# Kernel optimization log

Hardware: AMD Instinct MI355X
Metric: run time of the kernel (lower is better)

## Reference

```python
import jax, jax.numpy as jnp
import numpy as np

C = 128      # in channels
CO = 64      # out channels
G = 32       # group-norm groups
RES_IN = 32  # input resolution
RES_OUT = 64 # subdivided resolution
N = 20000    # active input voxels
EPS = 1e-5


def setup_inputs() -> dict:
    key = jax.random.key(0)
    ks = jax.random.split(key, 12)
    # unique active voxel coords at RES_IN (batch index 0, single instance)
    rng = np.random.default_rng(0)
    flat = rng.choice(RES_IN ** 3, size=N, replace=False)
    xyz = np.stack([flat // (RES_IN * RES_IN), (flat // RES_IN) % RES_IN, flat % RES_IN], axis=1)
    x_coords = jnp.asarray(np.concatenate([np.zeros((N, 1), np.int32), xyz.astype(np.int32)], axis=1))
    x_feats = jax.random.normal(ks[0], (N, C), dtype=jnp.float32)
    gn1_g = 1.0 + 0.1 * jax.random.normal(ks[1], (C,), dtype=jnp.float32)
    gn1_b = 0.1 * jax.random.normal(ks[2], (C,), dtype=jnp.float32)
    W1 = 0.05 * jax.random.normal(ks[3], (3, 3, 3, C, CO), dtype=jnp.float32)
    b1 = 0.01 * jax.random.normal(ks[4], (CO,), dtype=jnp.float32)
    gn2_g = 1.0 + 0.1 * jax.random.normal(ks[5], (CO,), dtype=jnp.float32)
    gn2_b = 0.1 * jax.random.normal(ks[6], (CO,), dtype=jnp.float32)
    W2 = 0.05 * jax.random.normal(ks[7], (3, 3, 3, CO, CO), dtype=jnp.float32)  # zero_module in source; random here to exercise math
    b2 = 0.01 * jax.random.normal(ks[8], (CO,), dtype=jnp.float32)
    Ws = 0.05 * jax.random.normal(ks[9], (C, CO), dtype=jnp.float32)   # 1x1 skip conv
    bs = 0.01 * jax.random.normal(ks[10], (CO,), dtype=jnp.float32)
    return dict(x_feats=x_feats, x_coords=x_coords, gn1_g=gn1_g, gn1_b=gn1_b,
                W1=W1, b1=b1, gn2_g=gn2_g, gn2_b=gn2_b, W2=W2, b2=b2, Ws=Ws, bs=bs)


def group_norm(f, g, b):
    # single-instance sparse group norm: stats per group over all points
    n, c = f.shape
    x = f.reshape(n, G, c // G)
    mu = jnp.mean(x, axis=(0, 2), keepdims=True)
    var = jnp.mean((x - mu) ** 2, axis=(0, 2), keepdims=True)
    return ((x - mu) * jax.lax.rsqrt(var + EPS)).reshape(n, c) * g + b


def subdivide(coords, feats):
    n = coords.shape[0]
    offs = jnp.stack(jnp.meshgrid(jnp.arange(2), jnp.arange(2), jnp.arange(2), indexing='ij'), -1).reshape(8, 3)
    xyz = coords[:, None, 1:] * 2 + offs[None].astype(coords.dtype)          # [n,8,3]
    bidx = jnp.broadcast_to(coords[:, None, :1], (n, 8, 1))
    new_coords = jnp.concatenate([bidx, xyz], axis=-1).reshape(n * 8, 4)
    return new_coords, jnp.repeat(feats, 8, axis=0)


def subm_conv3(coords, feats, W, b):
    # submanifold 3x3x3 sparse conv: scatter to padded dense grid, gather 27 neighbors per active site
    cin = feats.shape[1]
    grid = jnp.zeros((RES_OUT + 2, RES_OUT + 2, RES_OUT + 2, cin), feats.dtype)
    grid = grid.at[coords[:, 1] + 1, coords[:, 2] + 1, coords[:, 3] + 1].set(feats)
    acc = jnp.zeros((feats.shape[0], W.shape[-1]), feats.dtype)
    for i in range(3):
        for j in range(3):
            for k in range(3):
                nb = grid[coords[:, 1] + i, coords[:, 2] + j, coords[:, 3] + k]  # [n, cin]
                acc = acc + nb @ W[i, j, k]
    return acc + b


def reference(x_feats, x_coords, gn1_g, gn1_b, W1, b1, gn2_g, gn2_b, W2, b2, Ws, bs):
    h = jax.nn.silu(group_norm(x_feats, gn1_g, gn1_b))
    hc, hf = subdivide(x_coords, h)
    _, xf = subdivide(x_coords, x_feats)
    hf = subm_conv3(hc, hf, W1, b1)
    hf = jax.nn.silu(group_norm(hf, gn2_g, gn2_b))
    hf = subm_conv3(hc, hf, W2, b2)
    out = hf + (xf @ Ws + bs)  # residual + 1x1 skip conv (out_channels != channels)
    return out
```

## Files before the change

### kernel.cpp

```cpp
#include <hip/hip_runtime.h>
#include <hip/hip_bf16.h>
#include <math.h>

#define N_PTS 20000
#define C_IN 128
#define C_OUT 64
#define M_PTS (N_PTS*8)
#define EPS 1e-5f

typedef __attribute__((ext_vector_type(8))) short short8;
typedef __attribute__((ext_vector_type(4))) float float4v;

__device__ __forceinline__ ushort f2bf(float f){
    unsigned int i = __float_as_uint(f);
    unsigned int r = i + 0x7fffu + ((i >> 16) & 1u);
    return (ushort)(r >> 16);
}
__device__ __forceinline__ float bf2f(ushort u){ return __uint_as_float(((unsigned int)u) << 16); }
__device__ __forceinline__ float silu(float z){ return z / (1.f + expf(-z)); }


__global__ void __launch_bounds__(256) prep_kernel(
    const float* __restrict__ W1, const float* __restrict__ W2,
    ushort* __restrict__ Wt1, ushort* __restrict__ Wt2,
    int* __restrict__ pg, ushort* __restrict__ h, ushort* __restrict__ h2,
    const float* __restrict__ x, float* __restrict__ stats)
{
    const int b = blockIdx.x, tid = threadIdx.x;
    if (b < 2048){
        int idx = b * 256 + tid;
        int j = idx & 7, l = (idx >> 3) & 63, nb = (idx >> 9) & 3, kb = (idx >> 11) & 3, t = idx >> 13;
        int ci = kb * 32 + (l >> 4) * 8 + j, co = nb * 16 + (l & 15);
        int o = t >> 3, jj = t & 7;
        int ox = (o >> 2) & 1, oy = (o >> 1) & 1, oz = o & 1;
        int jx = (jj >> 2) & 1, jy = (jj >> 1) & 1, jz = jj & 1;
        float s = 0.f;
#pragma unroll
        for (int dx = -1; dx <= 1; dx++){
            if (((ox + dx) >> 1) != ox + jx - 1) continue;
#pragma unroll
            for (int dy = -1; dy <= 1; dy++){
                if (((oy + dy) >> 1) != oy + jy - 1) continue;
#pragma unroll
                for (int dz = -1; dz <= 1; dz++){
                    if (((oz + dz) >> 1) != oz + jz - 1) continue;
                    s += W1[((dx+1)*9 + (dy+1)*3 + (dz+1)) * (C_IN*64) + ci * 64 + co];
                }
            }
        }
        Wt1[idx] = f2bf(s);
    } else if (b < 2480){
        int idx = (b - 2048) * 256 + tid;
        int j = idx & 7, l = (idx >> 3) & 63, nb = (idx >> 9) & 3, kb = (idx >> 11) & 1, t = idx >> 12;
        int ci = kb * 32 + (l >> 4) * 8 + j, co = nb * 16 + (l & 15);
        Wt2[idx] = f2bf(W2[(t * C_OUT + ci) * 64 + co]);
    } else if (b < 2608){
        int i = (b - 2480) * 256 + tid;
        pg[i] = -1;
        if (b == 2480){
            if (tid < C_IN) h[(size_t)N_PTS * C_IN + tid] = 0;
            if (tid < 256){
                h2[(size_t)M_PTS * C_OUT + tid] = 0;
                h2[(size_t)M_PTS * C_OUT + 256 + tid] = 0;
            }
        }
    } else {
        __shared__ float ls[64];
        if (tid < 64) ls[tid] = 0.f;
        __syncthreads();
        const int g = tid & 31;
        const int r0 = (b - 2608) * 8 + (tid >> 5);
        float sum = 0.f, sq = 0.f;
        for (int r = r0; r < N_PTS; r += 4096){
            float4 v = *(const float4*)(x + (size_t)r * C_IN + g * 4);
            sum += v.x + v.y + v.z + v.w;
            sq  += v.x*v.x + v.y*v.y + v.z*v.z + v.w*v.w;
        }
        atomicAdd(&ls[g], sum);
        atomicAdd(&ls[32 + g], sq);
        __syncthreads();
        if (tid < 64) atomicAdd(&stats[tid], ls[tid]);
    }
}

__global__ void __launch_bounds__(256) mid_kernel(
    const int* __restrict__ cds, int* __restrict__ pg,
    const float* __restrict__ x, const float* __restrict__ stats,
    const float* __restrict__ g1, const float* __restrict__ b1, ushort* __restrict__ h,
    const float* __restrict__ Wsk, const float* __restrict__ bsk, float* __restrict__ s)
{
    __shared__ float w[C_IN * C_OUT];
    const int b = blockIdx.x, tid = threadIdx.x;
    if (b < 79){
        int i = b * 256 + tid;
        if (i < N_PTS){
            const int* cd = cds + i * 4;
            pg[(cd[1] * 32 + cd[2]) * 32 + cd[3]] = i;
        }
    } else if (b < 2579){
        int i = ((b - 79) * 256 + tid) * 4;
        int c0 = i & (C_IN - 1);
        int g = c0 >> 2;
        float mu = stats[g] * (1.0f / (N_PTS * 4.0f));
        float var = stats[32 + g] * (1.0f / (N_PTS * 4.0f)) - mu * mu;
        float rs = rsqrtf(var + EPS);
        float4 v = *(const float4*)(x + i);
        ushort4 o;
        o.x = f2bf(silu((v.x - mu) * rs * g1[c0+0] + b1[c0+0]));
        o.y = f2bf(silu((v.y - mu) * rs * g1[c0+1] + b1[c0+1]));
        o.z = f2bf(silu((v.z - mu) * rs * g1[c0+2] + b1[c0+2]));
        o.w = f2bf(silu((v.w - mu) * rs * g1[c0+3] + b1[c0+3]));
        *(ushort4*)(h + i) = o;
    } else {
        for (int j = tid; j < C_IN * C_OUT; j += 256) w[j] = Wsk[j];
        __syncthreads();
        int co = tid & 63, pr = tid >> 6;
        int p = (b - 2579) * 4 + pr;
        const float* xr = x + (size_t)p * C_IN;
        float a = bsk[co];
        for (int cb = 0; cb < C_IN; cb += 4){
            float4 v = *(const float4*)(xr + cb);
            a += v.x * w[(cb+0)*64+co] + v.y * w[(cb+1)*64+co]
               + v.z * w[(cb+2)*64+co] + v.w * w[(cb+3)*64+co];
        }
        s[(size_t)p * C_OUT + co] = a;
    }
}

__global__ void __launch_bounds__(64, 3) conv1_corner(
    const ushort* __restrict__ feat, const int* __restrict__ pg,
    const int* __restrict__ coords, const ushort* __restrict__ Wt,
    const float* __restrict__ bias, ushort* __restrict__ hf1_bf,
    float* __restrict__ statsAcc)
{
    const int l = threadIdx.x;
    const int r16 = l & 15, qd = l >> 4;
    const int bx = blockIdx.x, o = blockIdx.y;

    int p = bx * 64 + l;
    int pc = p < N_PTS ? p : N_PTS - 1;
    int px = coords[pc*4+1], py = coords[pc*4+2], pz = coords[pc*4+3];
    int ex0 = px + ((o >> 2) & 1) - 1;
    int ey0 = py + ((o >> 1) & 1) - 1;
    int ez0 = pz + (o & 1) - 1;

    int rows8[8];
#pragma unroll
    for (int j = 0; j < 8; j++){
        int cx = ex0 + ((j >> 2) & 1), cy = ey0 + ((j >> 1) & 1), cz = ez0 + (j & 1);
        int row = N_PTS;
        if ((unsigned)cx < 32u && (unsigned)cy < 32u && (unsigned)cz < 32u){
            int pi = pg[cx * 1024 + cy * 32 + cz];
            if (pi >= 0) row = pi;
        }
        rows8[j] = row;
    }

    float4v acc[16];
#pragma unroll
    for (int c = 0; c < 16; c++) acc[c] = 0.f;

#pragma unroll
    for (int j = 0; j < 8; j++){
        int fr0 = __shfl(rows8[j],      r16, 64);
        int fr1 = __shfl(rows8[j], 16 + r16, 64);
        int fr2 = __shfl(rows8[j], 32 + r16, 64);
        int fr3 = __shfl(rows8[j], 48 + r16, 64);
        const ushort* a0 = feat + (size_t)fr0 * C_IN + qd * 8;
        const ushort* a1 = feat + (size_t)fr1 * C_IN + qd * 8;
        const ushort* a2 = feat + (size_t)fr2 * C_IN + qd * 8;
        const ushort* a3 = feat + (size_t)fr3 * C_IN + qd * 8;
        const ushort* wt = Wt + (size_t)(o * 8 + j) * 8192 + l * 8;
#pragma unroll
        for (int kb = 0; kb < 4; kb++){
            short8 b0 = *(const short8*)(wt + (kb*4+0)*512);
            short8 b1 = *(const short8*)(wt + (kb*4+1)*512);
            short8 b2 = *(const short8*)(wt + (kb*4+2)*512);
            short8 b3 = *(const short8*)(wt + (kb*4+3)*512);
            short8 av0 = *(const short8*)(a0 + kb*32);
            short8 av1 = *(const short8*)(a1 + kb*32);
            short8 av2 = *(const short8*)(a2 + kb*32);
            short8 av3 = *(const short8*)(a3 + kb*32);
            acc[0]  = __builtin_amdgcn_mfma_f32_16x16x32_bf16(av0, b0, acc[0],  0, 0, 0);
            acc[1]  = __builtin_amdgcn_mfma_f32_16x16x32_bf16(av0, b1, acc[1],  0, 0, 0);
            acc[2]  = __builtin_amdgcn_mfma_f32_16x16x32_bf16(av0, b2, acc[2],  0, 0, 0);
            acc[3]  = __builtin_amdgcn_mfma_f32_16x16x32_bf16(av0, b3, acc[3],  0, 0, 0);
            acc[4]  = __builtin_amdgcn_mfma_f32_16x16x32_bf16(av1, b0, acc[4],  0, 0, 0);
            acc[5]  = __builtin_amdgcn_mfma_f32_16x16x32_bf16(av1, b1, acc[5],  0, 0, 0);
            acc[6]  = __builtin_amdgcn_mfma_f32_16x16x32_bf16(av1, b2, acc[6],  0, 0, 0);
            acc[7]  = __builtin_amdgcn_mfma_f32_16x16x32_bf16(av1, b3, acc[7],  0, 0, 0);
            acc[8]  = __builtin_amdgcn_mfma_f32_16x16x32_bf16(av2, b0, acc[8],  0, 0, 0);
            acc[9]  = __builtin_amdgcn_mfma_f32_16x16x32_bf16(av2, b1, acc[9],  0, 0, 0);
            acc[10] = __builtin_amdgcn_mfma_f32_16x16x32_bf16(av2, b2, acc[10], 0, 0, 0);
            acc[11] = __builtin_amdgcn_mfma_f32_16x16x32_bf16(av2, b3, acc[11], 0, 0, 0);
            acc[12] = __builtin_amdgcn_mfma_f32_16x16x32_bf16(av3, b0, acc[12], 0, 0, 0);
            acc[13] = __builtin_amdgcn_mfma_f32_16x16x32_bf16(av3, b1, acc[13], 0, 0, 0);
            acc[14] = __builtin_amdgcn_mfma_f32_16x16x32_bf16(av3, b2, acc[14], 0, 0, 0);
            acc[15] = __builtin_amdgcn_mfma_f32_16x16x32_bf16(av3, b3, acc[15], 0, 0, 0);
        }
    }

    float bsv[4] = { bias[r16], bias[16 + r16], bias[32 + r16], bias[48 + r16] };
    float ps[4] = {0,0,0,0}, pq[4] = {0,0,0,0};
#pragma unroll
    for (int rb = 0; rb < 4; rb++)
#pragma unroll
        for (int nb = 0; nb < 4; nb++)
#pragma unroll
            for (int rg = 0; rg < 4; rg++){
                int pr = bx * 64 + rb * 16 + qd * 4 + rg;
                float v = acc[rb * 4 + nb][rg] + bsv[nb];
                if (pr < N_PTS){
                    hf1_bf[(size_t)(pr * 8 + o) * 64 + nb * 16 + r16] = f2bf(v);
                    ps[nb] += v; pq[nb] += v * v;
                }
            }
#pragma unroll
    for (int nb = 0; nb < 4; nb++){
        float s1 = ps[nb], s2 = pq[nb];
        s1 += __shfl_xor(s1, 16, 64); s2 += __shfl_xor(s2, 16, 64);
        s1 += __shfl_xor(s1, 32, 64); s2 += __shfl_xor(s2, 32, 64);
        if (qd == 0){
            atomicAdd(&statsAcc[64 + nb * 16 + r16], s1);
            atomicAdd(&statsAcc[128 + nb * 16 + r16], s2);
        }
    }
}

__global__ void __launch_bounds__(64, 3) conv2_corner(
    const ushort* __restrict__ feat, const int* __restrict__ pg,
    const int* __restrict__ coords, const ushort* __restrict__ Wt,
    const float* __restrict__ bias, const float* __restrict__ skip,
    float* __restrict__ out)
{
    const int l = threadIdx.x;
    const int r16 = l & 15, qd = l >> 4;
    const int bx = blockIdx.x, o = blockIdx.y;
    const int ox = (o >> 2) & 1, oy = (o >> 1) & 1, oz = o & 1;

    int p = bx * 64 + l;
    int pc = p < N_PTS ? p : N_PTS - 1;
    int px = coords[pc*4+1], py = coords[pc*4+2], pz = coords[pc*4+3];
    int ex0 = px + ox - 1, ey0 = py + oy - 1, ez0 = pz + oz - 1;

    int pb[8];
#pragma unroll
    for (int j = 0; j < 8; j++){
        int cx = ex0 + ((j >> 2) & 1), cy = ey0 + ((j >> 1) & 1), cz = ez0 + (j & 1);
        int base = M_PTS;
        if ((unsigned)cx < 32u && (unsigned)cy < 32u && (unsigned)cz < 32u){
            int pi = pg[cx * 1024 + cy * 32 + cz];
            if (pi >= 0) base = pi * 8;
        }
        pb[j] = base;
    }

    float4v acc[16];
#pragma unroll
    for (int c = 0; c < 16; c++) acc[c] = 0.f;

#pragma unroll
    for (int t = 0; t < 27; t++){
        const int dx = t / 9 - 1, dy = (t / 3) % 3 - 1, dz = t % 3 - 1;
        int sx = ox + dx, sy = oy + dy, sz = oz + dz;
        int jx = (sx >> 1) - ox + 1, jy = (sy >> 1) - oy + 1, jz = (sz >> 1) - oz + 1;
        int opi = (sx & 1) * 4 + (sy & 1) * 2 + (sz & 1);
        int m00 = jz ? pb[1] : pb[0];
        int m01 = jz ? pb[3] : pb[2];
        int m10 = jz ? pb[5] : pb[4];
        int m11 = jz ? pb[7] : pb[6];
        int n0 = jy ? m01 : m00;
        int n1 = jy ? m11 : m10;
        int row = (jx ? n1 : n0) + opi;
        int fr0 = __shfl(row,      r16, 64);
        int fr1 = __shfl(row, 16 + r16, 64);
        int fr2 = __shfl(row, 32 + r16, 64);
        int fr3 = __shfl(row, 48 + r16, 64);
        const ushort* a0 = feat + (size_t)fr0 * C_OUT + qd * 8;
        const ushort* a1 = feat + (size_t)fr1 * C_OUT + qd * 8;
        const ushort* a2 = feat + (size_t)fr2 * C_OUT + qd * 8;
        const ushort* a3 = feat + (size_t)fr3 * C_OUT + qd * 8;
        const ushort* wt = Wt + (size_t)t * 4096 + l * 8;
#pragma unroll
        for (int kb = 0; kb < 2; kb++){
            short8 b0 = *(const short8*)(wt + (kb*4+0)*512);
            short8 b1 = *(const short8*)(wt + (kb*4+1)*512);
            short8 b2 = *(const short8*)(wt + (kb*4+2)*512);
            short8 b3 = *(const short8*)(wt + (kb*4+3)*512);
            short8 av0 = *(const short8*)(a0 + kb*32);
            short8 av1 = *(const short8*)(a1 + kb*32);
            short8 av2 = *(const short8*)(a2 + kb*32);
            short8 av3 = *(const short8*)(a3 + kb*32);
            acc[0]  = __builtin_amdgcn_mfma_f32_16x16x32_bf16(av0, b0, acc[0],  0, 0, 0);
            acc[1]  = __builtin_amdgcn_mfma_f32_16x16x32_bf16(av0, b1, acc[1],  0, 0, 0);
            acc[2]  = __builtin_amdgcn_mfma_f32_16x16x32_bf16(av0, b2, acc[2],  0, 0, 0);
            acc[3]  = __builtin_amdgcn_mfma_f32_16x16x32_bf16(av0, b3, acc[3],  0, 0, 0);
            acc[4]  = __builtin_amdgcn_mfma_f32_16x16x32_bf16(av1, b0, acc[4],  0, 0, 0);
            acc[5]  = __builtin_amdgcn_mfma_f32_16x16x32_bf16(av1, b1, acc[5],  0, 0, 0);
            acc[6]  = __builtin_amdgcn_mfma_f32_16x16x32_bf16(av1, b2, acc[6],  0, 0, 0);
            acc[7]  = __builtin_amdgcn_mfma_f32_16x16x32_bf16(av1, b3, acc[7],  0, 0, 0);
            acc[8]  = __builtin_amdgcn_mfma_f32_16x16x32_bf16(av2, b0, acc[8],  0, 0, 0);
            acc[9]  = __builtin_amdgcn_mfma_f32_16x16x32_bf16(av2, b1, acc[9],  0, 0, 0);
            acc[10] = __builtin_amdgcn_mfma_f32_16x16x32_bf16(av2, b2, acc[10], 0, 0, 0);
            acc[11] = __builtin_amdgcn_mfma_f32_16x16x32_bf16(av2, b3, acc[11], 0, 0, 0);
            acc[12] = __builtin_amdgcn_mfma_f32_16x16x32_bf16(av3, b0, acc[12], 0, 0, 0);
            acc[13] = __builtin_amdgcn_mfma_f32_16x16x32_bf16(av3, b1, acc[13], 0, 0, 0);
            acc[14] = __builtin_amdgcn_mfma_f32_16x16x32_bf16(av3, b2, acc[14], 0, 0, 0);
            acc[15] = __builtin_amdgcn_mfma_f32_16x16x32_bf16(av3, b3, acc[15], 0, 0, 0);
        }
    }

    float bsv[4] = { bias[r16], bias[16 + r16], bias[32 + r16], bias[48 + r16] };
#pragma unroll
    for (int rb = 0; rb < 4; rb++)
#pragma unroll
        for (int rg = 0; rg < 4; rg++){
            int pr = bx * 64 + rb * 16 + qd * 4 + rg;
            if (pr < N_PTS){
                const float* sk = skip + (size_t)pr * 64;
#pragma unroll
                for (int nb = 0; nb < 4; nb++){
                    int co = nb * 16 + r16;
                    out[(size_t)(pr * 8 + o) * 64 + co] = acc[rb * 4 + nb][rg] + bsv[nb] + sk[co];
                }
            }
        }
}

__global__ void __launch_bounds__(256) h2_kernel(
    const ushort* __restrict__ hf1, const float* __restrict__ stats,
    const float* __restrict__ gg, const float* __restrict__ gb, ushort* __restrict__ h2)
{
    int i = (blockIdx.x * 256 + threadIdx.x) * 4;
    if (i >= M_PTS * C_OUT) return;
    int c0 = i & (C_OUT - 1);
    const float inv = 1.0f / (M_PTS * 2.0f);
    float muA = (stats[64 + c0] + stats[64 + c0 + 1]) * inv;
    float vA  = (stats[128 + c0] + stats[128 + c0 + 1]) * inv - muA * muA;
    float rsA = rsqrtf(vA + EPS);
    float muB = (stats[64 + c0 + 2] + stats[64 + c0 + 3]) * inv;
    float vB  = (stats[128 + c0 + 2] + stats[128 + c0 + 3]) * inv - muB * muB;
    float rsB = rsqrtf(vB + EPS);
    ushort4 u = *(const ushort4*)(hf1 + i);
    ushort4 o;
    o.x = f2bf(silu((bf2f(u.x) - muA) * rsA * gg[c0+0] + gb[c0+0]));
    o.y = f2bf(silu((bf2f(u.y) - muA) * rsA * gg[c0+1] + gb[c0+1]));
    o.z = f2bf(silu((bf2f(u.z) - muB) * rsB * gg[c0+2] + gb[c0+2]));
    o.w = f2bf(silu((bf2f(u.w) - muB) * rsB * gg[c0+3] + gb[c0+3]));
    *(ushort4*)(h2 + i) = o;
}

extern "C" void kernel_launch(void* const* d_in, const int* in_sizes, int n_in,
                              void* d_out, int out_size, void* d_ws, size_t ws_size,
                              hipStream_t stream){
    const float* x   = (const float*)d_in[0];
    const int*   cds = (const int*)  d_in[1];
    const float* g1  = (const float*)d_in[2];
    const float* b1  = (const float*)d_in[3];
    const float* W1  = (const float*)d_in[4];
    const float* bb1 = (const float*)d_in[5];
    const float* g2  = (const float*)d_in[6];
    const float* b2  = (const float*)d_in[7];
    const float* W2  = (const float*)d_in[8];
    const float* bb2 = (const float*)d_in[9];
    const float* Wsk = (const float*)d_in[10];
    const float* bsk = (const float*)d_in[11];
    float* out = (float*)d_out;
    char* ws = (char*)d_ws;

    float*  stats = (float*) (ws);
    int*    pg    = (int*)   (ws + 1024);
    ushort* h     = (ushort*)(ws + 132096);
    ushort* h2    = (ushort*)(ws + 5252352);
    float*  s     = (float*) (ws + 25733376);
    ushort* Wt1   = (ushort*)(ws + 30853376);
    ushort* Wt2   = (ushort*)(ws + 31901952);

    hipMemsetAsync(stats, 0, 192 * sizeof(float), stream);
    prep_kernel<<<3120, 256, 0, stream>>>(W1, W2, Wt1, Wt2, pg, h, h2, x, stats);
    mid_kernel<<<7579, 256, 0, stream>>>(cds, pg, x, stats, g1, b1, h, Wsk, bsk, s);
    conv1_corner<<<dim3(313, 8), 64, 0, stream>>>(h, pg, cds, Wt1, bb1,
                                                  (ushort*)d_out, stats);
    h2_kernel<<<12500, 256, 0, stream>>>((const ushort*)d_out, stats, g2, b2, h2);
    conv2_corner<<<dim3(313, 8), 64, 0, stream>>>(h2, pg, cds, Wt2, bb2, s, out);
}
```

Measured before the change: 352.7 us.

## Halve conv tile to 32 points and remap blocks per XCD for L2 locality

Each conv wavefront now handles 32 points instead of 64, so the accumulators drop from 16 to 8 float4 vectors. The launch bound rises from 3 to 5 waves per EU to raise occupancy and hide gather latency. Block indices are remapped so that each of the 8 XCDs gets a contiguous range of tiles with all 8 octants, meant to improve L2 reuse of neighbour features and weights. Since 625 × 32 equals exactly 20000, the bounds checks are removed. The trade-off is that every weight load now feeds half as many MFMAs, so weight traffic per point doubles.

```diff
diff --git a/kernel.cpp b/kernel.cpp
--- a/kernel.cpp
+++ b/kernel.cpp
@@ -127,7 +127,7 @@
     }
 }
 
-__global__ void __launch_bounds__(64, 3) conv1_corner(
+__global__ void __launch_bounds__(64, 5) conv1_corner(
     const ushort* __restrict__ feat, const int* __restrict__ pg,
     const int* __restrict__ coords, const ushort* __restrict__ Wt,
     const float* __restrict__ bias, ushort* __restrict__ hf1_bf,
@@ -135,11 +135,13 @@
 {
     const int l = threadIdx.x;
     const int r16 = l & 15, qd = l >> 4;
-    const int bx = blockIdx.x, o = blockIdx.y;
-
-    int p = bx * 64 + l;
-    int pc = p < N_PTS ? p : N_PTS - 1;
-    int px = coords[pc*4+1], py = coords[pc*4+2], pz = coords[pc*4+3];
+    const int wg = blockIdx.x;
+    const int xcd = wg & 7, k = wg >> 3;
+    const int tile = xcd * 80 + (k >> 3), o = k & 7;
+    if (tile >= 625) return;
+
+    const int p = tile * 32 + (l & 31);
+    int px = coords[p*4+1], py = coords[p*4+2], pz = coords[p*4+3];
     int ex0 = px + ((o >> 2) & 1) - 1;
     int ey0 = py + ((o >> 1) & 1) - 1;
     int ez0 = pz + (o & 1) - 1;
@@ -156,20 +158,16 @@
         rows8[j] = row;
     }
 
-    float4v acc[16];
-#pragma unroll
-    for (int c = 0; c < 16; c++) acc[c] = 0.f;
+    float4v acc[8];
+#pragma unroll
+    for (int c = 0; c < 8; c++) acc[c] = 0.f;
 
 #pragma unroll
     for (int j = 0; j < 8; j++){
         int fr0 = __shfl(rows8[j],      r16, 64);
         int fr1 = __shfl(rows8[j], 16 + r16, 64);
-        int fr2 = __shfl(rows8[j], 32 + r16, 64);
-        int fr3 = __shfl(rows8[j], 48 + r16, 64);
         const ushort* a0 = feat + (size_t)fr0 * C_IN + qd * 8;
         const ushort* a1 = feat + (size_t)fr1 * C_IN + qd * 8;
-        const ushort* a2 = feat + (size_t)fr2 * C_IN + qd * 8;
-        const ushort* a3 = feat + (size_t)fr3 * C_IN + qd * 8;
         const ushort* wt = Wt + (size_t)(o * 8 + j) * 8192 + l * 8;
 #pragma unroll
         for (int kb = 0; kb < 4; kb++){
@@ -179,41 +177,29 @@
             short8 b3 = *(const short8*)(wt + (kb*4+3)*512);
             short8 av0 = *(const short8*)(a0 + kb*32);
             short8 av1 = *(const short8*)(a1 + kb*32);
-            short8 av2 = *(const short8*)(a2 + kb*32);
-            short8 av3 = *(const short8*)(a3 + kb*32);
-            acc[0]  = __builtin_amdgcn_mfma_f32_16x16x32_bf16(av0, b0, acc[0],  0, 0, 0);
-            acc[1]  = __builtin_amdgcn_mfma_f32_16x16x32_bf16(av0, b1, acc[1],  0, 0, 0);
-            acc[2]  = __builtin_amdgcn_mfma_f32_16x16x32_bf16(av0, b2, acc[2],  0, 0, 0);
-            acc[3]  = __builtin_amdgcn_mfma_f32_16x16x32_bf16(av0, b3, acc[3],  0, 0, 0);
-            acc[4]  = __builtin_amdgcn_mfma_f32_16x16x32_bf16(av1, b0, acc[4],  0, 0, 0);
-            acc[5]  = __builtin_amdgcn_mfma_f32_16x16x32_bf16(av1, b1, acc[5],  0, 0, 0);
-            acc[6]  = __builtin_amdgcn_mfma_f32_16x16x32_bf16(av1, b2, acc[6],  0, 0, 0);
-            acc[7]  = __builtin_amdgcn_mfma_f32_16x16x32_bf16(av1, b3, acc[7],  0, 0, 0);
-            acc[8]  = __builtin_amdgcn_mfma_f32_16x16x32_bf16(av2, b0, acc[8],  0, 0, 0);
-            acc[9]  = __builtin_amdgcn_mfma_f32_16x16x32_bf16(av2, b1, acc[9],  0, 0, 0);
-            acc[10] = __builtin_amdgcn_mfma_f32_16x16x32_bf16(av2, b2, acc[10], 0, 0, 0);
-            acc[11] = __builtin_amdgcn_mfma_f32_16x16x32_bf16(av2, b3, acc[11], 0, 0, 0);
-            acc[12] = __builtin_amdgcn_mfma_f32_16x16x32_bf16(av3, b0, acc[12], 0, 0, 0);
-            acc[13] = __builtin_amdgcn_mfma_f32_16x16x32_bf16(av3, b1, acc[13], 0, 0, 0);
-            acc[14] = __builtin_amdgcn_mfma_f32_16x16x32_bf16(av3, b2, acc[14], 0, 0, 0);
-            acc[15] = __builtin_amdgcn_mfma_f32_16x16x32_bf16(av3, b3, acc[15], 0, 0, 0);
+            acc[0] = __builtin_amdgcn_mfma_f32_16x16x32_bf16(av0, b0, acc[0], 0, 0, 0);
+            acc[1] = __builtin_amdgcn_mfma_f32_16x16x32_bf16(av0, b1, acc[1], 0, 0, 0);
+            acc[2] = __builtin_amdgcn_mfma_f32_16x16x32_bf16(av0, b2, acc[2], 0, 0, 0);
+            acc[3] = __builtin_amdgcn_mfma_f32_16x16x32_bf16(av0, b3, acc[3], 0, 0, 0);
+            acc[4] = __builtin_amdgcn_mfma_f32_16x16x32_bf16(av1, b0, acc[4], 0, 0, 0);
+            acc[5] = __builtin_amdgcn_mfma_f32_16x16x32_bf16(av1, b1, acc[5], 0, 0, 0);
+            acc[6] = __builtin_amdgcn_mfma_f32_16x16x32_bf16(av1, b2, acc[6], 0, 0, 0);
+            acc[7] = __builtin_amdgcn_mfma_f32_16x16x32_bf16(av1, b3, acc[7], 0, 0, 0);
         }
     }
 
     float bsv[4] = { bias[r16], bias[16 + r16], bias[32 + r16], bias[48 + r16] };
     float ps[4] = {0,0,0,0}, pq[4] = {0,0,0,0};
 #pragma unroll
-    for (int rb = 0; rb < 4; rb++)
+    for (int rb = 0; rb < 2; rb++)
 #pragma unroll
         for (int nb = 0; nb < 4; nb++)
 #pragma unroll
             for (int rg = 0; rg < 4; rg++){
-                int pr = bx * 64 + rb * 16 + qd * 4 + rg;
+                int pr = tile * 32 + rb * 16 + qd * 4 + rg;
                 float v = acc[rb * 4 + nb][rg] + bsv[nb];
-                if (pr < N_PTS){
-                    hf1_bf[(size_t)(pr * 8 + o) * 64 + nb * 16 + r16] = f2bf(v);
-                    ps[nb] += v; pq[nb] += v * v;
-                }
+                hf1_bf[(size_t)(pr * 8 + o) * 64 + nb * 16 + r16] = f2bf(v);
+                ps[nb] += v; pq[nb] += v * v;
             }
 #pragma unroll
     for (int nb = 0; nb < 4; nb++){
@@ -227,7 +213,7 @@
     }
 }
 
-__global__ void __launch_bounds__(64, 3) conv2_corner(
+__global__ void __launch_bounds__(64, 5) conv2_corner(
     const ushort* __restrict__ feat, const int* __restrict__ pg,
     const int* __restrict__ coords, const ushort* __restrict__ Wt,
     const float* __restrict__ bias, const float* __restrict__ skip,
@@ -235,12 +221,14 @@
 {
     const int l = threadIdx.x;
     const int r16 = l & 15, qd = l >> 4;
-    const int bx = blockIdx.x, o = blockIdx.y;
+    const int wg = blockIdx.x;
+    const int xcd = wg & 7, k = wg >> 3;
+    const int tile = xcd * 80 + (k >> 3), o = k & 7;
+    if (tile >= 625) return;
     const int ox = (o >> 2) & 1, oy = (o >> 1) & 1, oz = o & 1;
 
-    int p = bx * 64 + l;
-    int pc = p < N_PTS ? p : N_PTS - 1;
-    int px = coords[pc*4+1], py = coords[pc*4+2], pz = coords[pc*4+3];
+    const int p = tile * 32 + (l & 31);
+    int px = coords[p*4+1], py = coords[p*4+2], pz = coords[p*4+3];
     int ex0 = px + ox - 1, ey0 = py + oy - 1, ez0 = pz + oz - 1;
 
     int pb[8];
@@ -255,9 +243,9 @@
         pb[j] = base;
     }
 
-    float4v acc[16];
-#pragma unroll
-    for (int c = 0; c < 16; c++) acc[c] = 0.f;
+    float4v acc[8];
+#pragma unroll
+    for (int c = 0; c < 8; c++) acc[c] = 0.f;
 
 #pragma unroll
     for (int t = 0; t < 27; t++){
@@ -274,12 +262,8 @@
         int row = (jx ? n1 : n0) + opi;
         int fr0 = __shfl(row,      r16, 64);
         int fr1 = __shfl(row, 16 + r16, 64);
-        int fr2 = __shfl(row, 32 + r16, 64);
-        int fr3 = __shfl(row, 48 + r16, 64);
         const ushort* a0 = feat + (size_t)fr0 * C_OUT + qd * 8;
         const ushort* a1 = feat + (size_t)fr1 * C_OUT + qd * 8;
-        const ushort* a2 = feat + (size_t)fr2 * C_OUT + qd * 8;
-        const ushort* a3 = feat + (size_t)fr3 * C_OUT + qd * 8;
         const ushort* wt = Wt + (size_t)t * 4096 + l * 8;
 #pragma unroll
         for (int kb = 0; kb < 2; kb++){
@@ -289,40 +273,28 @@
             short8 b3 = *(const short8*)(wt + (kb*4+3)*512);
             short8 av0 = *(const short8*)(a0 + kb*32);
             short8 av1 = *(const short8*)(a1 + kb*32);
-            short8 av2 = *(const short8*)(a2 + kb*32);
-            short8 av3 = *(const short8*)(a3 + kb*32);
-            acc[0]  = __builtin_amdgcn_mfma_f32_16x16x32_bf16(av0, b0, acc[0],  0, 0, 0);
-            acc[1]  = __builtin_amdgcn_mfma_f32_16x16x32_bf16(av0, b1, acc[1],  0, 0, 0);
-            acc[2]  = __builtin_amdgcn_mfma_f32_16x16x32_bf16(av0, b2, acc[2],  0, 0, 0);
-            acc[3]  = __builtin_amdgcn_mfma_f32_16x16x32_bf16(av0, b3, acc[3],  0, 0, 0);
-            acc[4]  = __builtin_amdgcn_mfma_f32_16x16x32_bf16(av1, b0, acc[4],  0, 0, 0);
-            acc[5]  = __builtin_amdgcn_mfma_f32_16x16x32_bf16(av1, b1, acc[5],  0, 0, 0);
-            acc[6]  = __builtin_amdgcn_mfma_f32_16x16x32_bf16(av1, b2, acc[6],  0, 0, 0);
-            acc[7]  = __builtin_amdgcn_mfma_f32_16x16x32_bf16(av1, b3, acc[7],  0, 0, 0);
-            acc[8]  = __builtin_amdgcn_mfma_f32_16x16x32_bf16(av2, b0, acc[8],  0, 0, 0);
-            acc[9]  = __builtin_amdgcn_mfma_f32_16x16x32_bf16(av2, b1, acc[9],  0, 0, 0);
-            acc[10] = __builtin_amdgcn_mfma_f32_16x16x32_bf16(av2, b2, acc[10], 0, 0, 0);
-            acc[11] = __builtin_amdgcn_mfma_f32_16x16x32_bf16(av2, b3, acc[11], 0, 0, 0);
-            acc[12] = __builtin_amdgcn_mfma_f32_16x16x32_bf16(av3, b0, acc[12], 0, 0, 0);
-            acc[13] = __builtin_amdgcn_mfma_f32_16x16x32_bf16(av3, b1, acc[13], 0, 0, 0);
-            acc[14] = __builtin_amdgcn_mfma_f32_16x16x32_bf16(av3, b2, acc[14], 0, 0, 0);
-            acc[15] = __builtin_amdgcn_mfma_f32_16x16x32_bf16(av3, b3, acc[15], 0, 0, 0);
+            acc[0] = __builtin_amdgcn_mfma_f32_16x16x32_bf16(av0, b0, acc[0], 0, 0, 0);
+            acc[1] = __builtin_amdgcn_mfma_f32_16x16x32_bf16(av0, b1, acc[1], 0, 0, 0);
+            acc[2] = __builtin_amdgcn_mfma_f32_16x16x32_bf16(av0, b2, acc[2], 0, 0, 0);
+            acc[3] = __builtin_amdgcn_mfma_f32_16x16x32_bf16(av0, b3, acc[3], 0, 0, 0);
+            acc[4] = __builtin_amdgcn_mfma_f32_16x16x32_bf16(av1, b0, acc[4], 0, 0, 0);
+            acc[5] = __builtin_amdgcn_mfma_f32_16x16x32_bf16(av1, b1, acc[5], 0, 0, 0);
+            acc[6] = __builtin_amdgcn_mfma_f32_16x16x32_bf16(av1, b2, acc[6], 0, 0, 0);
+            acc[7] = __builtin_amdgcn_mfma_f32_16x16x32_bf16(av1, b3, acc[7], 0, 0, 0);
         }
     }
 
     float bsv[4] = { bias[r16], bias[16 + r16], bias[32 + r16], bias[48 + r16] };
 #pragma unroll
-    for (int rb = 0; rb < 4; rb++)
+    for (int rb = 0; rb < 2; rb++)
 #pragma unroll
         for (int rg = 0; rg < 4; rg++){
-            int pr = bx * 64 + rb * 16 + qd * 4 + rg;
-            if (pr < N_PTS){
-                const float* sk = skip + (size_t)pr * 64;
-#pragma unroll
-                for (int nb = 0; nb < 4; nb++){
-                    int co = nb * 16 + r16;
-                    out[(size_t)(pr * 8 + o) * 64 + co] = acc[rb * 4 + nb][rg] + bsv[nb] + sk[co];
-                }
+            int pr = tile * 32 + rb * 16 + qd * 4 + rg;
+            const float* sk = skip + (size_t)pr * 64;
+#pragma unroll
+            for (int nb = 0; nb < 4; nb++){
+                int co = nb * 16 + r16;
+                out[(size_t)(pr * 8 + o) * 64 + co] = acc[rb * 4 + nb][rg] + bsv[nb] + sk[co];
             }
         }
 }
@@ -379,8 +351,7 @@
     hipMemsetAsync(stats, 0, 192 * sizeof(float), stream);
     prep_kernel<<<3120, 256, 0, stream>>>(W1, W2, Wt1, Wt2, pg, h, h2, x, stats);
     mid_kernel<<<7579, 256, 0, stream>>>(cds, pg, x, stats, g1, b1, h, Wsk, bsk, s);
-    conv1_corner<<<dim3(313, 8), 64, 0, stream>>>(h, pg, cds, Wt1, bb1,
-                                                  (ushort*)d_out, stats);
+    conv1_corner<<<5120, 64, 0, stream>>>(h, pg, cds, Wt1, bb1, (ushort*)d_out, stats);
     h2_kernel<<<12500, 256, 0, stream>>>((const ushort*)d_out, stats, g2, b2, h2);
-    conv2_corner<<<dim3(313, 8), 64, 0, stream>>>(h2, pg, cds, Wt2, bb2, s, out);
-}
+    conv2_corner<<<5120, 64, 0, stream>>>(h2, pg, cds, Wt2, bb2, s, out);
+}
```

Result: slower. 415.5 us (+17.8%).
